# Optimization experiments

Measured on AMD Instinct MI355X. Metric: run time of the kernel, lower is better.

The kernel has to match this reference:

```python
import jax, jax.numpy as jnp
import numpy as np

EPS = 1e-5

def _mesh_conv_point(f, nbr, w, b):
    # f: [B, C, V] features; nbr: [B, V, K] neighbor vertex indices
    # gather neighbor features per batch: [B, C, V, K]
    g = jax.vmap(lambda fb, nb: fb[:, nb])(f, nbr)
    # prepend self feature -> [B, C, V, K+1]
    x = jnp.concatenate([f[:, :, :, None], g], axis=3)
    # Conv2d with kernel (1, K+1) == contraction over (C, K+1)
    return jnp.einsum('bcvk,ock->bov', x, w) + b[None, :, None]

def _instance_norm(y):
    # InstanceNorm2d (affine=False): normalize over spatial dims (V, 1)
    m = jnp.mean(y, axis=2, keepdims=True)
    v = jnp.var(y, axis=2, keepdims=True)
    return (y - m) * jax.lax.rsqrt(v + EPS)

def setup_inputs() -> dict:
    key = jax.random.key(0)
    k1, k2, k3, k4 = jax.random.split(key, 4)
    B, Cin, Cout, V, K = 4, 64, 128, 50000, 6
    fe = jax.random.normal(k1, (B, Cin, V), dtype=jnp.float32)
    nbrs = jax.random.randint(k2, (B, V, K), 0, V, dtype=jnp.int32)
    w1 = jax.random.normal(k3, (Cout, Cin, K + 1), dtype=jnp.float32) * (1.0 / np.sqrt(Cin * (K + 1)))
    b1 = jnp.zeros((Cout,), dtype=jnp.float32)
    w2 = jax.random.normal(k4, (Cout, Cout, K + 1), dtype=jnp.float32) * (1.0 / np.sqrt(Cout * (K + 1)))
    b2 = jnp.zeros((Cout,), dtype=jnp.float32)
    return {"fe": fe, "nbrs": nbrs, "w1": w1, "b1": b1, "w2": w2, "b2": b2}

def reference(fe, nbrs, w1, b1, w2, b2):
    # conv1 -> instance norm -> relu
    x1 = jax.nn.relu(_instance_norm(_mesh_conv_point(fe, nbrs, w1, b1)))
    # residual block: conv2 -> instance norm -> + x1 -> relu
    x2 = jax.nn.relu(_instance_norm(_mesh_conv_point(x1, nbrs, w2, b2)) + x1)
    # pool=0, so output == before_pool; return the single [B, Cout, V] tensor
    return x2
```

## Files before the change

kernel.cpp:

```cpp
#include <hip/hip_runtime.h>
#include <cstdint>
#include <cstddef>
#include <utility>

typedef unsigned short u16;
typedef u16 u16x8 __attribute__((ext_vector_type(8)));
typedef u16 u16x4 __attribute__((ext_vector_type(4)));
typedef _Float16 f16x8 __attribute__((ext_vector_type(8)));
typedef float f32x4 __attribute__((ext_vector_type(4)));

constexpr int B    = 4;
constexpr int CIN  = 64;
constexpr int COUT = 128;
constexpr int V    = 50000;
constexpr int KP1  = 7;
constexpr float EPS = 1e-5f;

constexpr int BN   = 128;
constexpr int NT   = (V + BN - 1) / BN;
constexpr int NTP  = 392;
constexpr int NT64 = (V + 63) / 64;

__device__ __forceinline__ u16 f2h(float f) {
    _Float16 h = (_Float16)f;
    return __builtin_bit_cast(u16, h);
}
__device__ __forceinline__ float h2f(u16 s) {
    return (float)__builtin_bit_cast(_Float16, s);
}

template<int... Is, typename F>
__device__ __forceinline__ void static_for_impl(F&& f, std::integer_sequence<int, Is...>) {
    (f(std::integral_constant<int, Is>{}), ...);
}
template<int N, typename F>
__device__ __forceinline__ void static_for(F&& f) {
    static_for_impl(f, std::make_integer_sequence<int, N>{});
}

template<int C>
__global__ __launch_bounds__(256) void prep_wf(const float* __restrict__ w,
                                               u16* __restrict__ wF) {
    constexpr int RCH = KP1 * C / 32;
    const int g = blockIdx.x * 256 + threadIdx.x;
    if (g >= RCH * 8 * 64) return;
    const int l  = g & 63;
    const int m  = (g >> 6) & 7;
    const int ch = g >> 9;
    const int k  = ch / (C / 32);
    const int c0 = (ch % (C / 32)) * 32;
    const int o  = m * 16 + (l & 15);
    u16x8 out;
#pragma unroll
    for (int j = 0; j < 8; ++j) {
        const int c = c0 + (l >> 4) * 8 + j;
        out[j] = f2h(w[((size_t)o * C + c) * KP1 + k]);
    }
    *(u16x8*)&wF[(size_t)g * 8] = out;
}

__global__ __launch_bounds__(256) void transpose_fe(const float* __restrict__ fe,
                                                    u16* __restrict__ feT) {
    __shared__ u16 tile[32][33];
    const int t  = threadIdx.x;
    const int tx = t & 31, ty = t >> 5;
    const int v0 = blockIdx.x * 32;
    const int c0 = blockIdx.y * 32;
    const int b  = blockIdx.z;
#pragma unroll
    for (int p = 0; p < 4; ++p) {
        const int c = c0 + ty + p * 8;
        const int v = v0 + tx;
        if (v < V) tile[ty + p * 8][tx] = f2h(fe[((size_t)b * CIN + c) * V + v]);
    }
    __syncthreads();
#pragma unroll
    for (int p = 0; p < 4; ++p) {
        const int v = v0 + ty + p * 8;
        const int c = c0 + tx;
        if (v < V) feT[((size_t)b * V + v) * CIN + c] = tile[tx][ty + p * 8];
    }
}

template<int C, int OUTL>
__global__ __launch_bounds__(256, 4) void conv_mfma(const u16* __restrict__ xin,
                                                    const u16* __restrict__ wF,
                                                    const float* __restrict__ bias,
                                                    const int*  __restrict__ nbr,
                                                    void* __restrict__ out_,
                                                    float2* __restrict__ P) {
    constexpr int NS = KP1 * C / 64;
    __shared__ __align__(16) u16 Xl[2][BN][72];
    float2* SredF = (float2*)&Xl[0][0][0];

    const int t    = threadIdx.x;
    const int b    = blockIdx.x / NT;
    const int tile = blockIdx.x % NT;
    const int v0   = tile * BN;
    const int w    = t >> 6;
    const int l    = t & 63;
    const int wo   = (w & 1) * 64;
    const int wv   = (w >> 1) * 64;

    const int sv = t >> 1;
    const int h  = t & 1;
    const int vS = v0 + sv;
    int idxS[KP1];
    {
        const int vc = (vS < V) ? vS : 0;
        idxS[0] = vc;
#pragma unroll
        for (int k = 1; k < KP1; ++k)
            idxS[k] = nbr[((size_t)b * V + vc) * 6 + (k - 1)];
    }

    int vn[4]; bool ok[4];
#pragma unroll
    for (int n = 0; n < 4; ++n) {
        vn[n] = v0 + wv + n * 16 + (l & 15);
        ok[n] = vn[n] < V;
    }

    f32x4 acc[4][4];
#pragma unroll
    for (int m = 0; m < 4; ++m)
#pragma unroll
        for (int n = 0; n < 4; ++n) acc[m][n] = (f32x4)0.f;

    u16x8 g[4];
    f16x8 af[8];

    auto gload = [&](auto SC) {
        constexpr int S    = decltype(SC)::value;
        constexpr int k_   = (C == 64) ? S : (S >> 1);
        constexpr int off_ = (C == 64) ? 0 : (S & 1) * 64;
        const u16* p_ = &xin[((size_t)b * V + idxS[k_]) * C + off_ + h * 32];
#pragma unroll
        for (int j = 0; j < 4; ++j) g[j] = *(const u16x8*)(p_ + j * 8);
    };
    auto aload = [&](auto SC) {
        constexpr int S = decltype(SC)::value;
#pragma unroll
        for (int kc = 0; kc < 2; ++kc)
#pragma unroll
            for (int m = 0; m < 4; ++m)
                af[kc * 4 + m] =
                    *(const f16x8*)&wF[(((size_t)(2 * S + kc) * 8 + (wo >> 4) + m) * 64 + l) * 8];
    };
    auto store = [&](int bufi) {
#pragma unroll
        for (int j = 0; j < 4; ++j)
            *(u16x8*)&Xl[bufi][sv][h * 32 + j * 8] = g[j];
    };

    gload(std::integral_constant<int, 0>{});
    store(0);
    asm volatile("s_waitcnt lgkmcnt(0)" ::: "memory");
    __builtin_amdgcn_s_barrier();

    static_for<NS>([&](auto SC) {
        constexpr int s = decltype(SC)::value;
        aload(SC);
        if constexpr (s + 1 < NS) gload(std::integral_constant<int, s + 1>{});
        f16x8 bf[4][2];
#pragma unroll
        for (int n = 0; n < 4; ++n)
#pragma unroll
            for (int kc = 0; kc < 2; ++kc)
                bf[n][kc] = *(const f16x8*)&Xl[s & 1][wv + n * 16 + (l & 15)]
                                              [kc * 32 + (l >> 4) * 8];
#pragma unroll
        for (int kc = 0; kc < 2; ++kc)
#pragma unroll
            for (int m = 0; m < 4; ++m)
#pragma unroll
                for (int n = 0; n < 4; ++n)
                    acc[m][n] = __builtin_amdgcn_mfma_f32_16x16x32_f16(af[kc * 4 + m],
                                                                       bf[n][kc],
                                                                       acc[m][n], 0, 0, 0);
        if constexpr (s + 1 < NS) {
            __builtin_amdgcn_sched_barrier(0);
            store((s + 1) & 1);
            asm volatile("s_waitcnt lgkmcnt(0)" ::: "memory");
            __builtin_amdgcn_s_barrier();
        }
    });

    if constexpr (OUTL == 0) {
        u16* po = (u16*)out_;
#pragma unroll
        for (int n = 0; n < 4; ++n) {
            if (ok[n]) {
#pragma unroll
                for (int m = 0; m < 4; ++m) {
                    const int o = wo + m * 16 + ((l >> 4) << 2);
                    u16x4 pk;
#pragma unroll
                    for (int q = 0; q < 4; ++q) pk[q] = f2h(acc[m][n][q] + bias[o + q]);
                    *(u16x4*)&po[((size_t)b * V + vn[n]) * COUT + o] = pk;
                }
            }
        }
    } else {
        float* po = (float*)out_;
#pragma unroll
        for (int m = 0; m < 4; ++m) {
            const int o = wo + m * 16 + ((l >> 4) << 2);
#pragma unroll
            for (int q = 0; q < 4; ++q) {
                const float bq = bias[o + q];
#pragma unroll
                for (int n = 0; n < 4; ++n)
                    if (ok[n]) po[((size_t)(b * COUT + o + q)) * V + vn[n]] = acc[m][n][q] + bq;
            }
        }
    }

    __syncthreads();

#pragma unroll
    for (int m = 0; m < 4; ++m) {
        const int o = wo + m * 16 + ((l >> 4) << 2);
        float s[4], s2[4];
#pragma unroll
        for (int q = 0; q < 4; ++q) {
            const float bq = bias[o + q];
            float a = 0.f, aa = 0.f;
#pragma unroll
            for (int n = 0; n < 4; ++n) {
                if (ok[n]) {
                    const float val = acc[m][n][q] + bq;
                    a += val; aa += val * val;
                }
            }
            s[q] = a; s2[q] = aa;
        }
#pragma unroll
        for (int d = 1; d < 16; d <<= 1) {
#pragma unroll
            for (int q = 0; q < 4; ++q) {
                s[q]  += __shfl_xor(s[q],  d, 16);
                s2[q] += __shfl_xor(s2[q], d, 16);
            }
        }
        if ((l & 15) == 0) {
#pragma unroll
            for (int q = 0; q < 4; ++q)
                SredF[w * COUT + o + q] = make_float2(s[q], s2[q]);
        }
    }
    __syncthreads();
    if (t < COUT) {
        const int wlo = t >> 6;
        const float2 a = SredF[wlo * COUT + t];
        const float2 c = SredF[(wlo + 2) * COUT + t];
        P[((size_t)b * COUT + t) * NTP + tile] = make_float2(a.x + c.x, a.y + c.y);
    }
}

__global__ __launch_bounds__(256) void finalize_fused(const float2* __restrict__ P,
                                                      float2* __restrict__ S) {
    const int row = blockIdx.x;
    float s = 0.f, s2 = 0.f;
    for (int i = threadIdx.x; i < NT; i += 256) {
        const float2 p = P[(size_t)row * NTP + i];
        s += p.x; s2 += p.y;
    }
    __shared__ float2 red[256];
    red[threadIdx.x] = make_float2(s, s2);
    __syncthreads();
    for (int w = 128; w > 0; w >>= 1) {
        if (threadIdx.x < w) {
            red[threadIdx.x].x += red[threadIdx.x + w].x;
            red[threadIdx.x].y += red[threadIdx.x + w].y;
        }
        __syncthreads();
    }
    if (threadIdx.x == 0) {
        const float m = red[0].x / V;
        const float var = red[0].y / V - m * m;
        S[row] = make_float2(m, rsqrtf(var + EPS));
    }
}

__global__ __launch_bounds__(256) void norm1(u16* __restrict__ x,
                                             const float2* __restrict__ S) {
    const unsigned e = ((unsigned)blockIdx.x * 256u + threadIdx.x) * 8u;
    if (e >= (unsigned)B * V * COUT) return;
    const unsigned b  = e / ((unsigned)V * COUT);
    const unsigned o0 = e & 127u;
    u16x8 vv = *(u16x8*)&x[e];
#pragma unroll
    for (int j = 0; j < 8; ++j) {
        const float2 s = S[b * COUT + o0 + j];
        float f = (h2f(vv[j]) - s.x) * s.y;
        vv[j] = f2h(fmaxf(f, 0.f));
    }
    *(u16x8*)&x[e] = vv;
}

__global__ __launch_bounds__(256) void final_mix2(const u16* __restrict__ y2,
                                                  const u16* __restrict__ x1,
                                                  const float2* __restrict__ S,
                                                  float* __restrict__ out) {
    __shared__ float ty[64][33], tx[64][33];
    const int t  = threadIdx.x;
    const int v0 = blockIdx.x * 64;
    const int o0 = blockIdx.y * 32;
    const int b  = blockIdx.z;
    const int jr = (t & 7) * 4;
    const int ir = t >> 3;
#pragma unroll
    for (int p = 0; p < 2; ++p) {
        const int i = ir + p * 32;
        const int v = v0 + i;
        if (v < V) {
            const size_t base = ((size_t)b * V + v) * COUT + o0 + jr;
            const u16x4 a = *(const u16x4*)&y2[base];
            const u16x4 c = *(const u16x4*)&x1[base];
#pragma unroll
            for (int q = 0; q < 4; ++q) {
                ty[i][jr + q] = h2f(a[q]);
                tx[i][jr + q] = h2f(c[q]);
            }
        }
    }
    __syncthreads();
    const int vl = t & 63, v = v0 + vl, oo0 = t >> 6;
    if (v < V) {
#pragma unroll
        for (int p = 0; p < 8; ++p) {
            const int oo = oo0 + p * 4;
            const int o  = o0 + oo;
            const float2 s = S[b * COUT + o];
            out[((size_t)b * COUT + o) * V + v] =
                fmaxf((ty[vl][oo] - s.x) * s.y + tx[vl][oo], 0.f);
        }
    }
}

__global__ __launch_bounds__(256) void final_mix(float* __restrict__ y,
                                                 const u16* __restrict__ x1,
                                                 const float2* __restrict__ S) {
    __shared__ float tile[64][33];
    const int t  = threadIdx.x;
    const int v0 = blockIdx.x * 64;
    const int o0 = blockIdx.y * 32;
    const int b  = blockIdx.z;
    const int j  = t & 31;
    const int i0 = t >> 5;
#pragma unroll
    for (int p = 0; p < 8; ++p) {
        const int i = i0 + p * 8;
        const int v = v0 + i;
        tile[i][j] = (v < V) ? h2f(x1[((size_t)b * V + v) * COUT + o0 + j]) : 0.f;
    }
    __syncthreads();
    const int vl  = t & 63;
    const int v   = v0 + vl;
    const int oo0 = t >> 6;
    if (v < V) {
#pragma unroll
        for (int p = 0; p < 8; ++p) {
            const int oo = oo0 + p * 4;
            const int o  = o0 + oo;
            const size_t idx = ((size_t)b * COUT + o) * V + v;
            const float2 s = S[b * COUT + o];
            const float f = (y[idx] - s.x) * s.y + tile[vl][oo];
            y[idx] = fmaxf(f, 0.f);
        }
    }
}

extern "C" void kernel_launch(void* const* d_in, const int* in_sizes, int n_in,
                              void* d_out, int out_size, void* d_ws, size_t ws_size,
                              hipStream_t stream) {
    const float* fe  = (const float*)d_in[0];
    const int*   nbr = (const int*)d_in[1];
    const float* w1  = (const float*)d_in[2];
    const float* b1  = (const float*)d_in[3];
    const float* w2  = (const float*)d_in[4];
    const float* b2  = (const float*)d_in[5];
    float* outf = (float*)d_out;
    char*  ws   = (char*)d_ws;

    constexpr size_t wF1_b = (size_t)(KP1 * CIN  / 32) * 8 * 64 * 8 * 2;
    constexpr size_t wF2_b = (size_t)(KP1 * COUT / 32) * 8 * 64 * 8 * 2;
    constexpr size_t S_b   = (size_t)B * COUT * 8;
    constexpr size_t Pf_b  = (size_t)B * COUT * NTP * 8;
    constexpr size_t x1_b  = (size_t)B * V * COUT * 2;
    constexpr size_t y2_b  = (size_t)B * V * COUT * 2;
    constexpr size_t feT_b = (size_t)B * V * CIN * 2;
    const size_t base = wF1_b + wF2_b + 2 * S_b + Pf_b;

    const bool full = (ws_size >= base + x1_b + y2_b);
    const bool t3   = (ws_size >= base + x1_b + feT_b);
    const bool t4   = (ws_size >= base + x1_b);
    if (!full && !t3 && !t4) return;

    size_t off = 0;
    u16*    wF1 = (u16*)(ws + off);    off += wF1_b;
    u16*    wF2 = (u16*)(ws + off);    off += wF2_b;
    float2* S1  = (float2*)(ws + off); off += S_b;
    float2* S2  = (float2*)(ws + off); off += S_b;
    float2* P   = (float2*)(ws + off); off += Pf_b;
    u16*    x1  = (u16*)(ws + off);    off += x1_b;
    u16*    ext = (u16*)(ws + off);

    u16* feT = (full || t3) ? ext : (u16*)d_out;

    prep_wf<CIN> <<<(KP1 * CIN  / 32) * 8 * 64 / 256, 256, 0, stream>>>(w1, wF1);
    prep_wf<COUT><<<(KP1 * COUT / 32) * 8 * 64 / 256, 256, 0, stream>>>(w2, wF2);

    dim3 gt((V + 31) / 32, CIN / 32, B);
    transpose_fe<<<gt, 256, 0, stream>>>(fe, feT);

    conv_mfma<CIN, 0><<<B * NT, 256, 0, stream>>>(feT, wF1, b1, nbr, x1, P);
    finalize_fused<<<B * COUT, 256, 0, stream>>>(P, S1);
    norm1<<<(int)((size_t)B * V * COUT / 8 / 256), 256, 0, stream>>>(x1, S1);

    dim3 gf(NT64, COUT / 32, B);
    if (full) {
        u16* y2 = ext;
        conv_mfma<COUT, 0><<<B * NT, 256, 0, stream>>>(x1, wF2, b2, nbr, y2, P);
        finalize_fused<<<B * COUT, 256, 0, stream>>>(P, S2);
        final_mix2<<<gf, 256, 0, stream>>>(y2, x1, S2, outf);
    } else {
        conv_mfma<COUT, 1><<<B * NT, 256, 0, stream>>>(x1, wF2, b2, nbr, outf, P);
        finalize_fused<<<B * COUT, 256, 0, stream>>>(P, S2);
        final_mix<<<gf, 256, 0, stream>>>(outf, x1, S2);
    }
}
```

Before: 241.8 us.

## Replace 4-wave conv tiles with single-wave 32-vertex tiles and nontemporal stores

Rewrites the gather-conv MFMA kernel so each 64-thread block (one wave) handles 32 vertices across all 128 output channels. Because only one wave shares the LDS buffer, workgroup barriers and the cross-wave reduction are no longer needed. Partial statistics per wave go straight to a larger P buffer, and finalize now sums over four times as many partials. Output stores in the conv and final-mix kernels become nontemporal. In exchange, weight fragments are reloaded by four times as many blocks and each wave carries less work to hide gather latency.

```diff
diff --git a/kernel.cpp b/kernel.cpp
--- a/kernel.cpp
+++ b/kernel.cpp
@@ -8,6 +8,7 @@
 typedef u16 u16x4 __attribute__((ext_vector_type(4)));
 typedef _Float16 f16x8 __attribute__((ext_vector_type(8)));
 typedef float f32x4 __attribute__((ext_vector_type(4)));
+typedef unsigned long long u64;
 
 constexpr int B    = 4;
 constexpr int CIN  = 64;
@@ -16,9 +17,8 @@
 constexpr int KP1  = 7;
 constexpr float EPS = 1e-5f;
 
-constexpr int BN   = 128;
-constexpr int NT   = (V + BN - 1) / BN;
-constexpr int NTP  = 392;
+constexpr int NTW  = (V + 31) / 32;
+constexpr int NTPW = 1568;
 constexpr int NT64 = (V + 63) / 64;
 
 __device__ __forceinline__ u16 f2h(float f) {
@@ -83,151 +83,126 @@
 }
 
 template<int C, int OUTL>
-__global__ __launch_bounds__(256, 4) void conv_mfma(const u16* __restrict__ xin,
-                                                    const u16* __restrict__ wF,
-                                                    const float* __restrict__ bias,
-                                                    const int*  __restrict__ nbr,
-                                                    void* __restrict__ out_,
-                                                    float2* __restrict__ P) {
-    constexpr int NS = KP1 * C / 64;
-    __shared__ __align__(16) u16 Xl[2][BN][72];
-    float2* SredF = (float2*)&Xl[0][0][0];
-
-    const int t    = threadIdx.x;
-    const int b    = blockIdx.x / NT;
-    const int tile = blockIdx.x % NT;
-    const int v0   = tile * BN;
-    const int w    = t >> 6;
-    const int l    = t & 63;
-    const int wo   = (w & 1) * 64;
-    const int wv   = (w >> 1) * 64;
-
-    const int sv = t >> 1;
-    const int h  = t & 1;
-    const int vS = v0 + sv;
+__global__ __launch_bounds__(64, 3) void conv_wave(const u16* __restrict__ xin,
+                                                   const u16* __restrict__ wF,
+                                                   const float* __restrict__ bias,
+                                                   const int*  __restrict__ nbr,
+                                                   void* __restrict__ out_,
+                                                   float2* __restrict__ P) {
+    constexpr int NS   = KP1 * C / 32;
+    constexpr int SPK  = C / 32;
+    constexpr int SMSK = SPK - 1;
+    __shared__ __align__(16) u16 Xl[2][32][40];
+
+    const int l  = threadIdx.x;
+    const int b  = blockIdx.x / NTW;
+    const int tw = blockIdx.x % NTW;
+    const int v0 = tw * 32;
+
+    const int sv = l >> 1;
+    const int h  = l & 1;
     int idxS[KP1];
     {
-        const int vc = (vS < V) ? vS : 0;
+        const int vc = (v0 + sv < V) ? (v0 + sv) : 0;
         idxS[0] = vc;
 #pragma unroll
         for (int k = 1; k < KP1; ++k)
             idxS[k] = nbr[((size_t)b * V + vc) * 6 + (k - 1)];
     }
 
-    int vn[4]; bool ok[4];
-#pragma unroll
-    for (int n = 0; n < 4; ++n) {
-        vn[n] = v0 + wv + n * 16 + (l & 15);
+    int vn[2]; bool ok[2];
+#pragma unroll
+    for (int n = 0; n < 2; ++n) {
+        vn[n] = v0 + n * 16 + (l & 15);
         ok[n] = vn[n] < V;
     }
 
-    f32x4 acc[4][4];
-#pragma unroll
-    for (int m = 0; m < 4; ++m)
-#pragma unroll
-        for (int n = 0; n < 4; ++n) acc[m][n] = (f32x4)0.f;
-
-    u16x8 g[4];
-    f16x8 af[8];
-
+    f32x4 acc[8][2];
+#pragma unroll
+    for (int m = 0; m < 8; ++m)
+#pragma unroll
+        for (int n = 0; n < 2; ++n) acc[m][n] = (f32x4)0.f;
+
+    u16x8 g[2];
     auto gload = [&](auto SC) {
-        constexpr int S    = decltype(SC)::value;
-        constexpr int k_   = (C == 64) ? S : (S >> 1);
-        constexpr int off_ = (C == 64) ? 0 : (S & 1) * 64;
-        const u16* p_ = &xin[((size_t)b * V + idxS[k_]) * C + off_ + h * 32];
-#pragma unroll
-        for (int j = 0; j < 4; ++j) g[j] = *(const u16x8*)(p_ + j * 8);
-    };
-    auto aload = [&](auto SC) {
-        constexpr int S = decltype(SC)::value;
-#pragma unroll
-        for (int kc = 0; kc < 2; ++kc)
-#pragma unroll
-            for (int m = 0; m < 4; ++m)
-                af[kc * 4 + m] =
-                    *(const f16x8*)&wF[(((size_t)(2 * S + kc) * 8 + (wo >> 4) + m) * 64 + l) * 8];
+        constexpr int S  = decltype(SC)::value;
+        constexpr int k_ = S / SPK;
+        constexpr int c0 = (S & SMSK) * 32;
+        const u16* p_ = &xin[((size_t)b * V + idxS[k_]) * C + c0 + h * 16];
+        g[0] = *(const u16x8*)(p_);
+        g[1] = *(const u16x8*)(p_ + 8);
     };
     auto store = [&](int bufi) {
-#pragma unroll
-        for (int j = 0; j < 4; ++j)
-            *(u16x8*)&Xl[bufi][sv][h * 32 + j * 8] = g[j];
+        *(u16x8*)&Xl[bufi][sv][h * 16]     = g[0];
+        *(u16x8*)&Xl[bufi][sv][h * 16 + 8] = g[1];
     };
 
     gload(std::integral_constant<int, 0>{});
     store(0);
-    asm volatile("s_waitcnt lgkmcnt(0)" ::: "memory");
-    __builtin_amdgcn_s_barrier();
 
     static_for<NS>([&](auto SC) {
         constexpr int s = decltype(SC)::value;
-        aload(SC);
+        f16x8 af[8];
+#pragma unroll
+        for (int m = 0; m < 8; ++m)
+            af[m] = *(const f16x8*)&wF[(((size_t)s * 8 + m) * 64 + l) * 8];
         if constexpr (s + 1 < NS) gload(std::integral_constant<int, s + 1>{});
-        f16x8 bf[4][2];
-#pragma unroll
-        for (int n = 0; n < 4; ++n)
-#pragma unroll
-            for (int kc = 0; kc < 2; ++kc)
-                bf[n][kc] = *(const f16x8*)&Xl[s & 1][wv + n * 16 + (l & 15)]
-                                              [kc * 32 + (l >> 4) * 8];
-#pragma unroll
-        for (int kc = 0; kc < 2; ++kc)
-#pragma unroll
-            for (int m = 0; m < 4; ++m)
-#pragma unroll
-                for (int n = 0; n < 4; ++n)
-                    acc[m][n] = __builtin_amdgcn_mfma_f32_16x16x32_f16(af[kc * 4 + m],
-                                                                       bf[n][kc],
-                                                                       acc[m][n], 0, 0, 0);
-        if constexpr (s + 1 < NS) {
-            __builtin_amdgcn_sched_barrier(0);
-            store((s + 1) & 1);
-            asm volatile("s_waitcnt lgkmcnt(0)" ::: "memory");
-            __builtin_amdgcn_s_barrier();
-        }
+        f16x8 bf[2];
+#pragma unroll
+        for (int n = 0; n < 2; ++n)
+            bf[n] = *(const f16x8*)&Xl[s & 1][n * 16 + (l & 15)][(l >> 4) * 8];
+#pragma unroll
+        for (int m = 0; m < 8; ++m)
+#pragma unroll
+            for (int n = 0; n < 2; ++n)
+                acc[m][n] = __builtin_amdgcn_mfma_f32_16x16x32_f16(af[m], bf[n],
+                                                                   acc[m][n], 0, 0, 0);
+        if constexpr (s + 1 < NS) store((s + 1) & 1);
     });
 
     if constexpr (OUTL == 0) {
         u16* po = (u16*)out_;
 #pragma unroll
-        for (int n = 0; n < 4; ++n) {
+        for (int n = 0; n < 2; ++n) {
             if (ok[n]) {
 #pragma unroll
-                for (int m = 0; m < 4; ++m) {
-                    const int o = wo + m * 16 + ((l >> 4) << 2);
+                for (int m = 0; m < 8; ++m) {
+                    const int o = m * 16 + ((l >> 4) << 2);
                     u16x4 pk;
 #pragma unroll
                     for (int q = 0; q < 4; ++q) pk[q] = f2h(acc[m][n][q] + bias[o + q]);
-                    *(u16x4*)&po[((size_t)b * V + vn[n]) * COUT + o] = pk;
+                    __builtin_nontemporal_store(*(const u64*)&pk,
+                        (u64*)&po[((size_t)b * V + vn[n]) * COUT + o]);
                 }
             }
         }
     } else {
         float* po = (float*)out_;
 #pragma unroll
-        for (int m = 0; m < 4; ++m) {
-            const int o = wo + m * 16 + ((l >> 4) << 2);
+        for (int m = 0; m < 8; ++m) {
+            const int o = m * 16 + ((l >> 4) << 2);
 #pragma unroll
             for (int q = 0; q < 4; ++q) {
                 const float bq = bias[o + q];
 #pragma unroll
-                for (int n = 0; n < 4; ++n)
-                    if (ok[n]) po[((size_t)(b * COUT + o + q)) * V + vn[n]] = acc[m][n][q] + bq;
+                for (int n = 0; n < 2; ++n)
+                    if (ok[n])
+                        __builtin_nontemporal_store(acc[m][n][q] + bq,
+                            &po[((size_t)(b * COUT + o + q)) * V + vn[n]]);
             }
         }
     }
 
-    __syncthreads();
-
-#pragma unroll
-    for (int m = 0; m < 4; ++m) {
-        const int o = wo + m * 16 + ((l >> 4) << 2);
+#pragma unroll
+    for (int m = 0; m < 8; ++m) {
+        const int o = m * 16 + ((l >> 4) << 2);
         float s[4], s2[4];
 #pragma unroll
         for (int q = 0; q < 4; ++q) {
             const float bq = bias[o + q];
             float a = 0.f, aa = 0.f;
 #pragma unroll
-            for (int n = 0; n < 4; ++n) {
+            for (int n = 0; n < 2; ++n) {
                 if (ok[n]) {
                     const float val = acc[m][n][q] + bq;
                     a += val; aa += val * val;
@@ -246,15 +221,8 @@
         if ((l & 15) == 0) {
 #pragma unroll
             for (int q = 0; q < 4; ++q)
-                SredF[w * COUT + o + q] = make_float2(s[q], s2[q]);
-        }
-    }
-    __syncthreads();
-    if (t < COUT) {
-        const int wlo = t >> 6;
-        const float2 a = SredF[wlo * COUT + t];
-        const float2 c = SredF[(wlo + 2) * COUT + t];
-        P[((size_t)b * COUT + t) * NTP + tile] = make_float2(a.x + c.x, a.y + c.y);
+                P[((size_t)b * COUT + o + q) * NTPW + tw] = make_float2(s[q], s2[q]);
+        }
     }
 }
 
@@ -262,8 +230,8 @@
                                                       float2* __restrict__ S) {
     const int row = blockIdx.x;
     float s = 0.f, s2 = 0.f;
-    for (int i = threadIdx.x; i < NT; i += 256) {
-        const float2 p = P[(size_t)row * NTP + i];
+    for (int i = threadIdx.x; i < NTW; i += 256) {
+        const float2 p = P[(size_t)row * NTPW + i];
         s += p.x; s2 += p.y;
     }
     __shared__ float2 red[256];
@@ -333,8 +301,9 @@
             const int oo = oo0 + p * 4;
             const int o  = o0 + oo;
             const float2 s = S[b * COUT + o];
-            out[((size_t)b * COUT + o) * V + v] =
-                fmaxf((ty[vl][oo] - s.x) * s.y + tx[vl][oo], 0.f);
+            __builtin_nontemporal_store(
+                fmaxf((ty[vl][oo] - s.x) * s.y + tx[vl][oo], 0.f),
+                &out[((size_t)b * COUT + o) * V + v]);
         }
     }
 }
@@ -387,7 +356,7 @@
     constexpr size_t wF1_b = (size_t)(KP1 * CIN  / 32) * 8 * 64 * 8 * 2;
     constexpr size_t wF2_b = (size_t)(KP1 * COUT / 32) * 8 * 64 * 8 * 2;
     constexpr size_t S_b   = (size_t)B * COUT * 8;
-    constexpr size_t Pf_b  = (size_t)B * COUT * NTP * 8;
+    constexpr size_t Pf_b  = (size_t)B * COUT * NTPW * 8;
     constexpr size_t x1_b  = (size_t)B * V * COUT * 2;
     constexpr size_t y2_b  = (size_t)B * V * COUT * 2;
     constexpr size_t feT_b = (size_t)B * V * CIN * 2;
@@ -415,18 +384,18 @@
     dim3 gt((V + 31) / 32, CIN / 32, B);
     transpose_fe<<<gt, 256, 0, stream>>>(fe, feT);
 
-    conv_mfma<CIN, 0><<<B * NT, 256, 0, stream>>>(feT, wF1, b1, nbr, x1, P);
+    conv_wave<CIN, 0><<<B * NTW, 64, 0, stream>>>(feT, wF1, b1, nbr, x1, P);
     finalize_fused<<<B * COUT, 256, 0, stream>>>(P, S1);
     norm1<<<(int)((size_t)B * V * COUT / 8 / 256), 256, 0, stream>>>(x1, S1);
 
     dim3 gf(NT64, COUT / 32, B);
     if (full) {
         u16* y2 = ext;
-        conv_mfma<COUT, 0><<<B * NT, 256, 0, stream>>>(x1, wF2, b2, nbr, y2, P);
+        conv_wave<COUT, 0><<<B * NTW, 64, 0, stream>>>(x1, wF2, b2, nbr, y2, P);
         finalize_fused<<<B * COUT, 256, 0, stream>>>(P, S2);
         final_mix2<<<gf, 256, 0, stream>>>(y2, x1, S2, outf);
     } else {
-        conv_mfma<COUT, 1><<<B * NT, 256, 0, stream>>>(x1, wF2, b2, nbr, outf, P);
+        conv_wave<COUT, 1><<<B * NTW, 64, 0, stream>>>(x1, wF2, b2, nbr, outf, P);
         finalize_fused<<<B * COUT, 256, 0, stream>>>(P, S2);
         final_mix<<<gf, 256, 0, stream>>>(outf, x1, S2);
     }
```

Measured after the change: 311.0 us. 1.29x slower.

## Fold first instance norm into conv2 weights and gather, dropping norm1 pass

Applied to the files above, without the earlier changes.

The separate norm1 pass, which read and rewrote the whole fp16 x1 tensor, is removed. The per-channel rsqrt scale is folded into per-batch copies of the conv2 weights. The mean subtraction and ReLU are applied in fp16 while gathered rows are staged into LDS, and the residual path recomputes the normalized x1 from the raw values in the final mix. The change also remaps block indices to interleave batches, and switches output writes to nontemporal stores. The cost is four weight copies, extra fp16 arithmetic in the gather, and a small precision shift from subtracting the mean in fp16.

```diff
diff --git a/kernel.cpp b/kernel.cpp
--- a/kernel.cpp
+++ b/kernel.cpp
@@ -8,6 +8,7 @@
 typedef u16 u16x4 __attribute__((ext_vector_type(4)));
 typedef _Float16 f16x8 __attribute__((ext_vector_type(8)));
 typedef float f32x4 __attribute__((ext_vector_type(4)));
+typedef unsigned long long u64;
 
 constexpr int B    = 4;
 constexpr int CIN  = 64;
@@ -27,6 +28,16 @@
 }
 __device__ __forceinline__ float h2f(u16 s) {
     return (float)__builtin_bit_cast(_Float16, s);
+}
+
+__device__ __forceinline__ void relusub8(u16x8& a, const u16x8& m) {
+    f16x8 af = __builtin_bit_cast(f16x8, a);
+    f16x8 mf = __builtin_bit_cast(f16x8, m);
+    f16x8 r = af - mf;
+#pragma unroll
+    for (int j = 0; j < 8; ++j)
+        r[j] = (r[j] > (_Float16)0.f) ? r[j] : (_Float16)0.f;
+    a = __builtin_bit_cast(u16x8, r);
 }
 
 template<int... Is, typename F>
@@ -59,6 +70,29 @@
     *(u16x8*)&wF[(size_t)g * 8] = out;
 }
 
+__global__ __launch_bounds__(256) void prep_wf_inv(const float* __restrict__ w,
+                                                   const float2* __restrict__ S1,
+                                                   u16* __restrict__ wF) {
+    constexpr int C = COUT;
+    constexpr int RCH = KP1 * C / 32;
+    const int g  = blockIdx.x * 256 + threadIdx.x;
+    const int bb = blockIdx.y;
+    if (g >= RCH * 8 * 64) return;
+    const int l  = g & 63;
+    const int m  = (g >> 6) & 7;
+    const int ch = g >> 9;
+    const int k  = ch / (C / 32);
+    const int c0 = (ch % (C / 32)) * 32;
+    const int o  = m * 16 + (l & 15);
+    u16x8 out;
+#pragma unroll
+    for (int j = 0; j < 8; ++j) {
+        const int c = c0 + (l >> 4) * 8 + j;
+        out[j] = f2h(w[((size_t)o * C + c) * KP1 + k] * S1[bb * COUT + c].y);
+    }
+    *(u16x8*)&wF[(size_t)bb * RCH * 8 * 64 * 8 + (size_t)g * 8] = out;
+}
+
 __global__ __launch_bounds__(256) void transpose_fe(const float* __restrict__ fe,
                                                     u16* __restrict__ feT) {
     __shared__ u16 tile[32][33];
@@ -82,25 +116,30 @@
     }
 }
 
-template<int C, int OUTL>
+template<int C, int OUTL, int NORM>
 __global__ __launch_bounds__(256, 4) void conv_mfma(const u16* __restrict__ xin,
                                                     const u16* __restrict__ wF,
                                                     const float* __restrict__ bias,
                                                     const int*  __restrict__ nbr,
+                                                    const u16*  __restrict__ mh,
                                                     void* __restrict__ out_,
                                                     float2* __restrict__ P) {
     constexpr int NS = KP1 * C / 64;
     __shared__ __align__(16) u16 Xl[2][BN][72];
     float2* SredF = (float2*)&Xl[0][0][0];
 
+    const int i    = blockIdx.x;
+    const int b    = (i & 7) >> 1;
+    const int tile = ((i >> 3) << 1) | (i & 1);
+    const int v0   = tile * BN;
     const int t    = threadIdx.x;
-    const int b    = blockIdx.x / NT;
-    const int tile = blockIdx.x % NT;
-    const int v0   = tile * BN;
     const int w    = t >> 6;
     const int l    = t & 63;
     const int wo   = (w & 1) * 64;
     const int wv   = (w >> 1) * 64;
+
+    if constexpr (NORM)
+        wF += (size_t)b * (KP1 * C / 32) * 8 * 64 * 8;
 
     const int sv = t >> 1;
     const int h  = t & 1;
@@ -114,6 +153,16 @@
             idxS[k] = nbr[((size_t)b * V + vc) * 6 + (k - 1)];
     }
 
+    u16x8 mreg[2][4];
+    if constexpr (NORM) {
+        const u16* mp = mh + b * COUT;
+#pragma unroll
+        for (int sel = 0; sel < 2; ++sel)
+#pragma unroll
+            for (int j = 0; j < 4; ++j)
+                mreg[sel][j] = *(const u16x8*)&mp[sel * 64 + h * 32 + j * 8];
+    }
+
     int vn[4]; bool ok[4];
 #pragma unroll
     for (int n = 0; n < 4; ++n) {
@@ -147,14 +196,19 @@
                 af[kc * 4 + m] =
                     *(const f16x8*)&wF[(((size_t)(2 * S + kc) * 8 + (wo >> 4) + m) * 64 + l) * 8];
     };
-    auto store = [&](int bufi) {
+    auto store = [&](int bufi, auto SC) {
+        if constexpr (NORM) {
+            constexpr int sel = decltype(SC)::value & 1;
+#pragma unroll
+            for (int j = 0; j < 4; ++j) relusub8(g[j], mreg[sel][j]);
+        }
 #pragma unroll
         for (int j = 0; j < 4; ++j)
             *(u16x8*)&Xl[bufi][sv][h * 32 + j * 8] = g[j];
     };
 
     gload(std::integral_constant<int, 0>{});
-    store(0);
+    store(0, std::integral_constant<int, 0>{});
     asm volatile("s_waitcnt lgkmcnt(0)" ::: "memory");
     __builtin_amdgcn_s_barrier();
 
@@ -180,7 +234,7 @@
                                                                        acc[m][n], 0, 0, 0);
         if constexpr (s + 1 < NS) {
             __builtin_amdgcn_sched_barrier(0);
-            store((s + 1) & 1);
+            store((s + 1) & 1, std::integral_constant<int, s + 1>{});
             asm volatile("s_waitcnt lgkmcnt(0)" ::: "memory");
             __builtin_amdgcn_s_barrier();
         }
@@ -197,7 +251,8 @@
                     u16x4 pk;
 #pragma unroll
                     for (int q = 0; q < 4; ++q) pk[q] = f2h(acc[m][n][q] + bias[o + q]);
-                    *(u16x4*)&po[((size_t)b * V + vn[n]) * COUT + o] = pk;
+                    __builtin_nontemporal_store(*(const u64*)&pk,
+                        (u64*)&po[((size_t)b * V + vn[n]) * COUT + o]);
                 }
             }
         }
@@ -211,7 +266,9 @@
                 const float bq = bias[o + q];
 #pragma unroll
                 for (int n = 0; n < 4; ++n)
-                    if (ok[n]) po[((size_t)(b * COUT + o + q)) * V + vn[n]] = acc[m][n][q] + bq;
+                    if (ok[n])
+                        __builtin_nontemporal_store(acc[m][n][q] + bq,
+                            &po[((size_t)(b * COUT + o + q)) * V + vn[n]]);
             }
         }
     }
@@ -259,7 +316,8 @@
 }
 
 __global__ __launch_bounds__(256) void finalize_fused(const float2* __restrict__ P,
-                                                      float2* __restrict__ S) {
+                                                      float2* __restrict__ S,
+                                                      u16* __restrict__ mh) {
     const int row = blockIdx.x;
     float s = 0.f, s2 = 0.f;
     for (int i = threadIdx.x; i < NT; i += 256) {
@@ -280,28 +338,14 @@
         const float m = red[0].x / V;
         const float var = red[0].y / V - m * m;
         S[row] = make_float2(m, rsqrtf(var + EPS));
-    }
-}
-
-__global__ __launch_bounds__(256) void norm1(u16* __restrict__ x,
-                                             const float2* __restrict__ S) {
-    const unsigned e = ((unsigned)blockIdx.x * 256u + threadIdx.x) * 8u;
-    if (e >= (unsigned)B * V * COUT) return;
-    const unsigned b  = e / ((unsigned)V * COUT);
-    const unsigned o0 = e & 127u;
-    u16x8 vv = *(u16x8*)&x[e];
-#pragma unroll
-    for (int j = 0; j < 8; ++j) {
-        const float2 s = S[b * COUT + o0 + j];
-        float f = (h2f(vv[j]) - s.x) * s.y;
-        vv[j] = f2h(fmaxf(f, 0.f));
-    }
-    *(u16x8*)&x[e] = vv;
+        if (mh) mh[row] = f2h(m);
+    }
 }
 
 __global__ __launch_bounds__(256) void final_mix2(const u16* __restrict__ y2,
-                                                  const u16* __restrict__ x1,
-                                                  const float2* __restrict__ S,
+                                                  const u16* __restrict__ y1,
+                                                  const float2* __restrict__ S1,
+                                                  const float2* __restrict__ S2,
                                                   float* __restrict__ out) {
     __shared__ float ty[64][33], tx[64][33];
     const int t  = threadIdx.x;
@@ -317,11 +361,12 @@
         if (v < V) {
             const size_t base = ((size_t)b * V + v) * COUT + o0 + jr;
             const u16x4 a = *(const u16x4*)&y2[base];
-            const u16x4 c = *(const u16x4*)&x1[base];
+            const u16x4 c = *(const u16x4*)&y1[base];
 #pragma unroll
             for (int q = 0; q < 4; ++q) {
+                const float2 s1 = S1[b * COUT + o0 + jr + q];
                 ty[i][jr + q] = h2f(a[q]);
-                tx[i][jr + q] = h2f(c[q]);
+                tx[i][jr + q] = s1.y * fmaxf(h2f(c[q]) - s1.x, 0.f);
             }
         }
     }
@@ -332,16 +377,18 @@
         for (int p = 0; p < 8; ++p) {
             const int oo = oo0 + p * 4;
             const int o  = o0 + oo;
-            const float2 s = S[b * COUT + o];
-            out[((size_t)b * COUT + o) * V + v] =
-                fmaxf((ty[vl][oo] - s.x) * s.y + tx[vl][oo], 0.f);
+            const float2 s = S2[b * COUT + o];
+            __builtin_nontemporal_store(
+                fmaxf((ty[vl][oo] - s.x) * s.y + tx[vl][oo], 0.f),
+                &out[((size_t)b * COUT + o) * V + v]);
         }
     }
 }
 
 __global__ __launch_bounds__(256) void final_mix(float* __restrict__ y,
-                                                 const u16* __restrict__ x1,
-                                                 const float2* __restrict__ S) {
+                                                 const u16* __restrict__ y1,
+                                                 const float2* __restrict__ S1,
+                                                 const float2* __restrict__ S2) {
     __shared__ float tile[64][33];
     const int t  = threadIdx.x;
     const int v0 = blockIdx.x * 64;
@@ -349,11 +396,14 @@
     const int b  = blockIdx.z;
     const int j  = t & 31;
     const int i0 = t >> 5;
+    const float2 s1 = S1[b * COUT + o0 + j];
 #pragma unroll
     for (int p = 0; p < 8; ++p) {
         const int i = i0 + p * 8;
         const int v = v0 + i;
-        tile[i][j] = (v < V) ? h2f(x1[((size_t)b * V + v) * COUT + o0 + j]) : 0.f;
+        tile[i][j] = (v < V)
+            ? s1.y * fmaxf(h2f(y1[((size_t)b * V + v) * COUT + o0 + j]) - s1.x, 0.f)
+            : 0.f;
     }
     __syncthreads();
     const int vl  = t & 63;
@@ -365,7 +415,7 @@
             const int oo = oo0 + p * 4;
             const int o  = o0 + oo;
             const size_t idx = ((size_t)b * COUT + o) * V + v;
-            const float2 s = S[b * COUT + o];
+            const float2 s = S2[b * COUT + o];
             const float f = (y[idx] - s.x) * s.y + tile[vl][oo];
             y[idx] = fmaxf(f, 0.f);
         }
@@ -385,13 +435,14 @@
     char*  ws   = (char*)d_ws;
 
     constexpr size_t wF1_b = (size_t)(KP1 * CIN  / 32) * 8 * 64 * 8 * 2;
-    constexpr size_t wF2_b = (size_t)(KP1 * COUT / 32) * 8 * 64 * 8 * 2;
+    constexpr size_t wF2_b = (size_t)B * (KP1 * COUT / 32) * 8 * 64 * 8 * 2;
     constexpr size_t S_b   = (size_t)B * COUT * 8;
+    constexpr size_t mh_b  = ((size_t)B * COUT * 2 + 255) & ~255ull;
     constexpr size_t Pf_b  = (size_t)B * COUT * NTP * 8;
     constexpr size_t x1_b  = (size_t)B * V * COUT * 2;
     constexpr size_t y2_b  = (size_t)B * V * COUT * 2;
     constexpr size_t feT_b = (size_t)B * V * CIN * 2;
-    const size_t base = wF1_b + wF2_b + 2 * S_b + Pf_b;
+    const size_t base = wF1_b + wF2_b + 2 * S_b + mh_b + Pf_b;
 
     const bool full = (ws_size >= base + x1_b + y2_b);
     const bool t3   = (ws_size >= base + x1_b + feT_b);
@@ -403,31 +454,33 @@
     u16*    wF2 = (u16*)(ws + off);    off += wF2_b;
     float2* S1  = (float2*)(ws + off); off += S_b;
     float2* S2  = (float2*)(ws + off); off += S_b;
+    u16*    mh1 = (u16*)(ws + off);    off += mh_b;
     float2* P   = (float2*)(ws + off); off += Pf_b;
     u16*    x1  = (u16*)(ws + off);    off += x1_b;
     u16*    ext = (u16*)(ws + off);
 
     u16* feT = (full || t3) ? ext : (u16*)d_out;
 
-    prep_wf<CIN> <<<(KP1 * CIN  / 32) * 8 * 64 / 256, 256, 0, stream>>>(w1, wF1);
-    prep_wf<COUT><<<(KP1 * COUT / 32) * 8 * 64 / 256, 256, 0, stream>>>(w2, wF2);
+    prep_wf<CIN><<<(KP1 * CIN / 32) * 8 * 64 / 256, 256, 0, stream>>>(w1, wF1);
 
     dim3 gt((V + 31) / 32, CIN / 32, B);
     transpose_fe<<<gt, 256, 0, stream>>>(fe, feT);
 
-    conv_mfma<CIN, 0><<<B * NT, 256, 0, stream>>>(feT, wF1, b1, nbr, x1, P);
-    finalize_fused<<<B * COUT, 256, 0, stream>>>(P, S1);
-    norm1<<<(int)((size_t)B * V * COUT / 8 / 256), 256, 0, stream>>>(x1, S1);
+    conv_mfma<CIN, 0, 0><<<B * NTP, 256, 0, stream>>>(feT, wF1, b1, nbr, nullptr, x1, P);
+    finalize_fused<<<B * COUT, 256, 0, stream>>>(P, S1, mh1);
+
+    dim3 gw((KP1 * COUT / 32) * 8 * 64 / 256, B);
+    prep_wf_inv<<<gw, 256, 0, stream>>>(w2, S1, wF2);
 
     dim3 gf(NT64, COUT / 32, B);
     if (full) {
         u16* y2 = ext;
-        conv_mfma<COUT, 0><<<B * NT, 256, 0, stream>>>(x1, wF2, b2, nbr, y2, P);
-        finalize_fused<<<B * COUT, 256, 0, stream>>>(P, S2);
-        final_mix2<<<gf, 256, 0, stream>>>(y2, x1, S2, outf);
+        conv_mfma<COUT, 0, 1><<<B * NTP, 256, 0, stream>>>(x1, wF2, b2, nbr, mh1, y2, P);
+        finalize_fused<<<B * COUT, 256, 0, stream>>>(P, S2, nullptr);
+        final_mix2<<<gf, 256, 0, stream>>>(y2, x1, S1, S2, outf);
     } else {
-        conv_mfma<COUT, 1><<<B * NT, 256, 0, stream>>>(x1, wF2, b2, nbr, outf, P);
-        finalize_fused<<<B * COUT, 256, 0, stream>>>(P, S2);
-        final_mix<<<gf, 256, 0, stream>>>(outf, x1, S2);
-    }
-}
+        conv_mfma<COUT, 1, 1><<<B * NTP, 256, 0, stream>>>(x1, wF2, b2, nbr, mh1, outf, P);
+        finalize_fused<<<B * COUT, 256, 0, stream>>>(P, S2, nullptr);
+        final_mix<<<gf, 256, 0, stream>>>(outf, x1, S1, S2);
+    }
+}
```

After: 276.6 us. 14.4% more time.
